# Kernel tuning notes

Hardware: AMD Instinct MI355X
Metric: run time of the kernel (lower is better)

## Reference

```python
import jax, jax.numpy as jnp
import numpy as np

B, N, F_IN, F_OUT = 16, 1024, 256, 256
ALPHA = 0.2  # leakyrelu negative slope
NEG_BIG = -9e15


def setup_inputs() -> dict:
    key = jax.random.key(0)
    k1, k2, k3, k4 = jax.random.split(key, 4)
    h = jax.random.normal(k1, (B, N, F_IN), dtype=jnp.float32)
    adj = jax.random.randint(k2, (B, N, N), 0, 2, dtype=jnp.int32)
    # xavier_uniform with gain=1.414
    def xavier(k, shape, gain=1.414):
        fan_in, fan_out = shape[0], shape[1]
        bound = gain * np.sqrt(6.0 / (fan_in + fan_out))
        return jax.random.uniform(k, shape, dtype=jnp.float32, minval=-bound, maxval=bound)
    W = xavier(k3, (F_IN, F_OUT))
    a = xavier(k4, (2 * F_OUT, 1))
    return {"h": h, "adj": adj, "W": W, "a": a}


def reference(h, adj, W, a):
    Wh = jnp.matmul(h, W)  # [B, N, F_OUT]
    # a^T [Wh_i ; Wh_j] = a1^T Wh_i + a2^T Wh_j -- avoids O(N^2 * 2F) concat tensor
    a1 = a[:F_OUT, 0]  # [F_OUT]
    a2 = a[F_OUT:, 0]  # [F_OUT]
    e_i = jnp.einsum('bnf,f->bn', Wh, a1)  # score contribution of source node i
    e_j = jnp.einsum('bnf,f->bn', Wh, a2)  # score contribution of target node j
    e = e_i[:, :, None] + e_j[:, None, :]  # [B, N, N]
    e = jnp.where(e > 0, e, ALPHA * e)  # leaky relu
    e = jnp.where(adj > 0, e, NEG_BIG)
    attention = jax.nn.softmax(e, axis=2)
    h_prime = jnp.matmul(attention, Wh)  # [B, N, F_OUT]
    return jax.nn.elu(h_prime)  # concat=True
```

## Files before the change

### kernel.cpp

```cpp
#include <hip/hip_runtime.h>
#include <hip/hip_bf16.h>

#define B_ 16
#define N_ 1024
#define F_ 256
#define ALPHA 0.2f
#define NEG_BIG -9.0e15f
#define LOG2E 1.4426950408889634f

typedef float f4 __attribute__((ext_vector_type(4)));
typedef float f32x4 __attribute__((ext_vector_type(4)));
typedef short s16x8 __attribute__((ext_vector_type(8)));
typedef short s16x4 __attribute__((ext_vector_type(4)));

__device__ inline short f2bs(float x) {
    __hip_bfloat16 h = __float2bfloat16(x);
    return __builtin_bit_cast(short, h);
}

__global__ __launch_bounds__(256) void k_pre(const float* __restrict__ W,
                                             const float* __restrict__ a,
                                             float* __restrict__ wa,
                                             unsigned short* __restrict__ WTb) {
    const int t = threadIdx.x, lane = t & 63, w = t >> 6;
    if (blockIdx.x < 64) {
        const int row = blockIdx.x * 4 + w;
        const f4 wv = *(const f4*)(W + (size_t)row * F_ + lane * 4);
        const f4 a1 = *(const f4*)(a + lane * 4);
        const f4 a2 = *(const f4*)(a + F_ + lane * 4);
        float s1 = wv[0]*a1[0] + wv[1]*a1[1] + wv[2]*a1[2] + wv[3]*a1[3];
        float s2 = wv[0]*a2[0] + wv[1]*a2[1] + wv[2]*a2[2] + wv[3]*a2[3];
#pragma unroll
        for (int off = 32; off > 0; off >>= 1) {
            s1 += __shfl_xor(s1, off);
            s2 += __shfl_xor(s2, off);
        }
        if (lane == 0) { wa[row] = s1; wa[256 + row] = s2; }
    } else {
        __shared__ float tile[64][65];
        const int wb = blockIdx.x - 64;
        const int k0 = (wb >> 2) * 64, f0 = (wb & 3) * 64;
#pragma unroll
        for (int rep = 0; rep < 4; ++rep) {
            const int idx = rep * 256 + t;
            const int kr = idx >> 4, fc = (idx & 15) * 4;
            const f4 v = *(const f4*)(W + (size_t)(k0 + kr) * F_ + f0 + fc);
            tile[kr][fc] = v[0]; tile[kr][fc + 1] = v[1];
            tile[kr][fc + 2] = v[2]; tile[kr][fc + 3] = v[3];
        }
        __syncthreads();
#pragma unroll
        for (int rep = 0; rep < 4; ++rep) {
            const int idx = rep * 256 + t;
            const int fr = idx >> 4, kc = (idx & 15) * 4;
            s16x4 v;
            v[0] = f2bs(tile[kc][fr]);     v[1] = f2bs(tile[kc + 1][fr]);
            v[2] = f2bs(tile[kc + 2][fr]); v[3] = f2bs(tile[kc + 3][fr]);
            *(s16x4*)(WTb + (size_t)(f0 + fr) * F_ + k0 + kc) = v;
        }
    }
}

__global__ __launch_bounds__(256, 4) void k_big(const float* __restrict__ h,
                                                const unsigned short* __restrict__ WTb,
                                                const float* __restrict__ wa,
                                                const int* __restrict__ adj,
                                                unsigned short* __restrict__ WhT,
                                                float* __restrict__ ei,
                                                float* __restrict__ ej,
                                                unsigned long long* __restrict__ mask) {
    const int bid = blockIdx.x;
    const int t = threadIdx.x, l = t & 63, w = t >> 6;
    if (bid < 2048) {
        const int gw = bid * 4 + w;
#pragma unroll
        for (int rr = 0; rr < 2; ++rr) {
            const int row = gw + rr * 8192;
            const int* ar = adj + (size_t)row * 1024;
            int v[16];
#pragma unroll
            for (int g = 0; g < 16; ++g) v[g] = ar[g * 64 + l];
            unsigned long long myw = 0;
#pragma unroll
            for (int g = 0; g < 16; ++g) {
                const unsigned long long bal = __ballot(v[g] > 0);
                if (l == g) myw = bal;
            }
            if (l < 16) mask[(size_t)row * 16 + l] = myw;
        }
    } else if (bid < 2560) {
        const int m0 = (bid - 2048) * 32;
        const int ih = w >> 1, fh = w & 1;
        const int li = l & 15, jg = l >> 4;
        const int mrow = m0 + ih * 16 + li;
        const float* hrow = h + (size_t)mrow * F_ + jg * 8;
        const unsigned short* bbase = WTb + (size_t)(fh * 128 + li) * F_ + jg * 8;
        f32x4 acc[8] = {};
#pragma unroll
        for (int kk = 0; kk < 8; ++kk) {
            const f4 lo = *(const f4*)(hrow + kk * 32);
            const f4 hi = *(const f4*)(hrow + kk * 32 + 4);
            s16x8 av;
            av[0]=f2bs(lo[0]); av[1]=f2bs(lo[1]); av[2]=f2bs(lo[2]); av[3]=f2bs(lo[3]);
            av[4]=f2bs(hi[0]); av[5]=f2bs(hi[1]); av[6]=f2bs(hi[2]); av[7]=f2bs(hi[3]);
#pragma unroll
            for (int ft = 0; ft < 8; ++ft) {
                const s16x8 bv = *(const s16x8*)(bbase + (size_t)ft * 16 * F_ + kk * 32);
                acc[ft] = __builtin_amdgcn_mfma_f32_16x16x32_bf16(av, bv, acc[ft], 0, 0, 0);
            }
        }
        const int bb = m0 >> 10;
        const int mb = (m0 & 1023) + ih * 16 + jg * 4;
#pragma unroll
        for (int ft = 0; ft < 8; ++ft) {
            const int fg = fh * 128 + ft * 16 + li;
            s16x4 v;
            v[0]=f2bs(acc[ft][0]); v[1]=f2bs(acc[ft][1]);
            v[2]=f2bs(acc[ft][2]); v[3]=f2bs(acc[ft][3]);
            *(s16x4*)(WhT + ((size_t)(bb * 256 + fg)) * 1024 + mb) = v;
        }
    } else {
        const int row = (bid - 2560) * 4 + w;
        const f4 hv = *(const f4*)(h + (size_t)row * F_ + l * 4);
        const f4 w1 = *(const f4*)(wa + l * 4);
        const f4 w2 = *(const f4*)(wa + 256 + l * 4);
        float s1 = hv[0]*w1[0] + hv[1]*w1[1] + hv[2]*w1[2] + hv[3]*w1[3];
        float s2 = hv[0]*w2[0] + hv[1]*w2[1] + hv[2]*w2[2] + hv[3]*w2[3];
#pragma unroll
        for (int off = 32; off > 0; off >>= 1) {
            s1 += __shfl_xor(s1, off);
            s2 += __shfl_xor(s2, off);
        }
        if (l == 0) { ei[row] = s1 * LOG2E; ej[row] = s2 * LOG2E; }
    }
}

__global__ __launch_bounds__(256, 2) void k_attn(const unsigned short* __restrict__ WhT,
                                                 const float* __restrict__ ei_g,
                                                 const float* __restrict__ ej_g,
                                                 const unsigned long long* __restrict__ mask,
                                                 float* __restrict__ out) {
    const int id = blockIdx.x;
    const int xcd = id & 7, slot = id >> 3;
    const int b = xcd * 2 + (slot >> 5);
    const int i0 = (slot & 31) * 32;

    const int t = threadIdx.x, l = t & 63, w = t >> 6;
    const int fbase = w * 64;
    const int li = l & 15, jg = l >> 4;

    const unsigned short* whb = WhT + (size_t)b * F_ * N_;
    const float* ejb = ej_g + b * N_;
    const float ei0 = ei_g[b * N_ + i0 + li];
    const float ei1 = ei_g[b * N_ + i0 + 16 + li];
    const unsigned long long* mrow0 = mask + (size_t)(b * N_ + i0 + li) * 16;
    const unsigned long long* mrow1 = mrow0 + 256;

    const unsigned short* bptr[4];
#pragma unroll
    for (int ft = 0; ft < 4; ++ft)
        bptr[ft] = whb + (size_t)(fbase + ft * 16 + li) * N_ + jg * 8;

    float m0 = NEG_BIG, m1 = NEG_BIG, ll0 = 0.f, ll1 = 0.f;
    f32x4 acc0[4] = {}, acc1[4] = {};

    for (int s = 0; s < 16; ++s) {
        const unsigned long long w0 = mrow0[s], w1 = mrow1[s];
        const int jb = s * 64 + jg * 8;
        const f4 ejA = *(const f4*)(ejb + jb);
        const f4 ejB = *(const f4*)(ejb + jb + 4);
        const f4 ejC = *(const f4*)(ejb + jb + 32);
        const f4 ejD = *(const f4*)(ejb + jb + 36);
        s16x8 bv0[4], bv1[4];
#pragma unroll
        for (int ft = 0; ft < 4; ++ft) {
            bv0[ft] = *(const s16x8*)(bptr[ft] + s * 64);
            bv1[ft] = *(const s16x8*)(bptr[ft] + s * 64 + 32);
        }
#pragma unroll
        for (int sub = 0; sub < 2; ++sub) {
            const f4 eja = sub ? ejC : ejA;
            const f4 ejbv = sub ? ejD : ejB;
            const unsigned int ms0 = (unsigned int)(w0 >> (sub * 32 + jg * 8));
            const unsigned int ms1 = (unsigned int)(w1 >> (sub * 32 + jg * 8));
            float p0[8], p1[8];
            float tm0 = NEG_BIG, tm1 = NEG_BIG;
#pragma unroll
            for (int e = 0; e < 8; ++e) {
                const float ejv = (e < 4) ? eja[e] : ejbv[e - 4];
                float s0 = ei0 + ejv;
                s0 = fmaxf(s0, ALPHA * s0);
                p0[e] = s0; tm0 = fmaxf(tm0, s0);
                float s1 = ei1 + ejv;
                s1 = fmaxf(s1, ALPHA * s1);
                p1[e] = s1; tm1 = fmaxf(tm1, s1);
            }
            tm0 = fmaxf(tm0, __shfl_xor(tm0, 16));
            tm0 = fmaxf(tm0, __shfl_xor(tm0, 32));
            tm1 = fmaxf(tm1, __shfl_xor(tm1, 16));
            tm1 = fmaxf(tm1, __shfl_xor(tm1, 32));
            if (__any(tm0 > m0 + 11.5f)) {
                const float mn = fmaxf(m0, tm0);
                const float fac = __builtin_amdgcn_exp2f(m0 - mn);
                m0 = mn; ll0 *= fac;
                float fr[4];
#pragma unroll
                for (int q = 0; q < 4; ++q) fr[q] = __shfl(fac, jg * 4 + q);
#pragma unroll
                for (int ft = 0; ft < 4; ++ft)
#pragma unroll
                    for (int q = 0; q < 4; ++q) acc0[ft][q] *= fr[q];
            }
            if (__any(tm1 > m1 + 11.5f)) {
                const float mn = fmaxf(m1, tm1);
                const float fac = __builtin_amdgcn_exp2f(m1 - mn);
                m1 = mn; ll1 *= fac;
                float fr[4];
#pragma unroll
                for (int q = 0; q < 4; ++q) fr[q] = __shfl(fac, jg * 4 + q);
#pragma unroll
                for (int ft = 0; ft < 4; ++ft)
#pragma unroll
                    for (int q = 0; q < 4; ++q) acc1[ft][q] *= fr[q];
            }
            float sum0 = 0.f, sum1 = 0.f;
            s16x8 af0, af1;
#pragma unroll
            for (int e = 0; e < 8; ++e) {
                const float b0 = (float)((ms0 >> e) & 1u);
                const float b1 = (float)((ms1 >> e) & 1u);
                const float pe0 = __builtin_amdgcn_exp2f(p0[e] - m0) * b0;
                const float pe1 = __builtin_amdgcn_exp2f(p1[e] - m1) * b1;
                af0[e] = f2bs(pe0); sum0 += pe0;
                af1[e] = f2bs(pe1); sum1 += pe1;
            }
            sum0 += __shfl_xor(sum0, 16); sum0 += __shfl_xor(sum0, 32);
            sum1 += __shfl_xor(sum1, 16); sum1 += __shfl_xor(sum1, 32);
            ll0 += sum0; ll1 += sum1;
            const s16x8* bv = sub ? bv1 : bv0;
#pragma unroll
            for (int ft = 0; ft < 4; ++ft) {
                acc0[ft] = __builtin_amdgcn_mfma_f32_16x16x32_bf16(af0, bv[ft], acc0[ft], 0, 0, 0);
                acc1[ft] = __builtin_amdgcn_mfma_f32_16x16x32_bf16(af1, bv[ft], acc1[ft], 0, 0, 0);
            }
        }
    }

    const float il0 = 1.f / ll0, il1 = 1.f / ll1;
    float inv0[4], inv1[4];
#pragma unroll
    for (int q = 0; q < 4; ++q) {
        inv0[q] = __shfl(il0, jg * 4 + q);
        inv1[q] = __shfl(il1, jg * 4 + q);
    }
#pragma unroll
    for (int ft = 0; ft < 4; ++ft) {
#pragma unroll
        for (int q = 0; q < 4; ++q) {
            float v0 = acc0[ft][q] * inv0[q];
            v0 = v0 > 0.f ? v0 : __builtin_amdgcn_exp2f(v0 * LOG2E) - 1.f;
            out[((size_t)b * N_ + i0 + jg * 4 + q) * F_ + fbase + ft * 16 + li] = v0;
            float v1 = acc1[ft][q] * inv1[q];
            v1 = v1 > 0.f ? v1 : __builtin_amdgcn_exp2f(v1 * LOG2E) - 1.f;
            out[((size_t)b * N_ + i0 + 16 + jg * 4 + q) * F_ + fbase + ft * 16 + li] = v1;
        }
    }
}

extern "C" void kernel_launch(void* const* d_in, const int* in_sizes, int n_in,
                              void* d_out, int out_size, void* d_ws, size_t ws_size,
                              hipStream_t stream) {
    const float* h = (const float*)d_in[0];
    const int* adj = (const int*)d_in[1];
    const float* W = (const float*)d_in[2];
    const float* a = (const float*)d_in[3];
    float* out = (float*)d_out;

    unsigned short* WhT = (unsigned short*)d_ws;
    float* wa = (float*)(WhT + (size_t)B_ * N_ * F_);
    float* ei = wa + 512;
    float* ej = ei + (size_t)B_ * N_;
    unsigned short* WTb = (unsigned short*)(ej + (size_t)B_ * N_);
    unsigned long long* mask = (unsigned long long*)(WTb + 65536);

    k_pre<<<80, 256, 0, stream>>>(W, a, wa, WTb);
    k_big<<<6656, 256, 0, stream>>>(h, WTb, wa, adj, WhT, ei, ej, mask);
    k_attn<<<512, 256, 0, stream>>>(WhT, ei, ej, mask, out);
}
```

Measured before the change: 188.2 us.

## Split softmax scoring across waves and share probabilities through LDS

The attention kernel now handles 16 query rows per block instead of 32, with twice as many blocks and a higher occupancy target. Each wave now computes scores, masked exponentials and row sums for 4 of the 16 rows rather than every wave redundantly computing all rows. The bf16 probability tile and the rescale factors are exchanged through shared memory before the MFMA accumulation. In exchange it adds two block barriers per 64-column step, rescales the accumulator unconditionally, and reloads WhT from global memory twice as often, since each block now covers fewer rows.

After: 202.6 us. 7.7% more time.

```diff
diff --git a/kernel.cpp b/kernel.cpp
--- a/kernel.cpp
+++ b/kernel.cpp
@@ -135,134 +135,105 @@
     }
 }
 
-__global__ __launch_bounds__(256, 2) void k_attn(const unsigned short* __restrict__ WhT,
+__global__ __launch_bounds__(256, 4) void k_attn(const unsigned short* __restrict__ WhT,
                                                  const float* __restrict__ ei_g,
                                                  const float* __restrict__ ej_g,
                                                  const unsigned long long* __restrict__ mask,
                                                  float* __restrict__ out) {
     const int id = blockIdx.x;
     const int xcd = id & 7, slot = id >> 3;
-    const int b = xcd * 2 + (slot >> 5);
-    const int i0 = (slot & 31) * 32;
+    const int b = xcd * 2 + (slot >> 6);
+    const int i0 = (slot & 63) * 16;
+
+    __shared__ unsigned short P_lds[16][72];
+    __shared__ __align__(16) float sF[16];
 
     const int t = threadIdx.x, l = t & 63, w = t >> 6;
+    const int li = l & 15, jg = l >> 4;
     const int fbase = w * 64;
-    const int li = l & 15, jg = l >> 4;
+
+    const int orow = w * 4 + jg;
+    const float eival = ei_g[b * N_ + i0 + orow];
+    const unsigned long long* mrow = mask + (size_t)(b * N_ + i0 + orow) * 16;
+    const float* ejb = ej_g + b * N_;
 
     const unsigned short* whb = WhT + (size_t)b * F_ * N_;
-    const float* ejb = ej_g + b * N_;
-    const float ei0 = ei_g[b * N_ + i0 + li];
-    const float ei1 = ei_g[b * N_ + i0 + 16 + li];
-    const unsigned long long* mrow0 = mask + (size_t)(b * N_ + i0 + li) * 16;
-    const unsigned long long* mrow1 = mrow0 + 256;
-
     const unsigned short* bptr[4];
 #pragma unroll
     for (int ft = 0; ft < 4; ++ft)
         bptr[ft] = whb + (size_t)(fbase + ft * 16 + li) * N_ + jg * 8;
 
-    float m0 = NEG_BIG, m1 = NEG_BIG, ll0 = 0.f, ll1 = 0.f;
-    f32x4 acc0[4] = {}, acc1[4] = {};
+    float m = NEG_BIG, ll = 0.f;
+    f32x4 acc[4] = {};
 
     for (int s = 0; s < 16; ++s) {
-        const unsigned long long w0 = mrow0[s], w1 = mrow1[s];
-        const int jb = s * 64 + jg * 8;
-        const f4 ejA = *(const f4*)(ejb + jb);
-        const f4 ejB = *(const f4*)(ejb + jb + 4);
-        const f4 ejC = *(const f4*)(ejb + jb + 32);
-        const f4 ejD = *(const f4*)(ejb + jb + 36);
         s16x8 bv0[4], bv1[4];
 #pragma unroll
         for (int ft = 0; ft < 4; ++ft) {
             bv0[ft] = *(const s16x8*)(bptr[ft] + s * 64);
             bv1[ft] = *(const s16x8*)(bptr[ft] + s * 64 + 32);
         }
-#pragma unroll
-        for (int sub = 0; sub < 2; ++sub) {
-            const f4 eja = sub ? ejC : ejA;
-            const f4 ejbv = sub ? ejD : ejB;
-            const unsigned int ms0 = (unsigned int)(w0 >> (sub * 32 + jg * 8));
-            const unsigned int ms1 = (unsigned int)(w1 >> (sub * 32 + jg * 8));
-            float p0[8], p1[8];
-            float tm0 = NEG_BIG, tm1 = NEG_BIG;
-#pragma unroll
-            for (int e = 0; e < 8; ++e) {
-                const float ejv = (e < 4) ? eja[e] : ejbv[e - 4];
-                float s0 = ei0 + ejv;
-                s0 = fmaxf(s0, ALPHA * s0);
-                p0[e] = s0; tm0 = fmaxf(tm0, s0);
-                float s1 = ei1 + ejv;
-                s1 = fmaxf(s1, ALPHA * s1);
-                p1[e] = s1; tm1 = fmaxf(tm1, s1);
-            }
-            tm0 = fmaxf(tm0, __shfl_xor(tm0, 16));
-            tm0 = fmaxf(tm0, __shfl_xor(tm0, 32));
-            tm1 = fmaxf(tm1, __shfl_xor(tm1, 16));
-            tm1 = fmaxf(tm1, __shfl_xor(tm1, 32));
-            if (__any(tm0 > m0 + 11.5f)) {
-                const float mn = fmaxf(m0, tm0);
-                const float fac = __builtin_amdgcn_exp2f(m0 - mn);
-                m0 = mn; ll0 *= fac;
-                float fr[4];
-#pragma unroll
-                for (int q = 0; q < 4; ++q) fr[q] = __shfl(fac, jg * 4 + q);
-#pragma unroll
-                for (int ft = 0; ft < 4; ++ft)
-#pragma unroll
-                    for (int q = 0; q < 4; ++q) acc0[ft][q] *= fr[q];
-            }
-            if (__any(tm1 > m1 + 11.5f)) {
-                const float mn = fmaxf(m1, tm1);
-                const float fac = __builtin_amdgcn_exp2f(m1 - mn);
-                m1 = mn; ll1 *= fac;
-                float fr[4];
-#pragma unroll
-                for (int q = 0; q < 4; ++q) fr[q] = __shfl(fac, jg * 4 + q);
-#pragma unroll
-                for (int ft = 0; ft < 4; ++ft)
-#pragma unroll
-                    for (int q = 0; q < 4; ++q) acc1[ft][q] *= fr[q];
-            }
-            float sum0 = 0.f, sum1 = 0.f;
-            s16x8 af0, af1;
-#pragma unroll
-            for (int e = 0; e < 8; ++e) {
-                const float b0 = (float)((ms0 >> e) & 1u);
-                const float b1 = (float)((ms1 >> e) & 1u);
-                const float pe0 = __builtin_amdgcn_exp2f(p0[e] - m0) * b0;
-                const float pe1 = __builtin_amdgcn_exp2f(p1[e] - m1) * b1;
-                af0[e] = f2bs(pe0); sum0 += pe0;
-                af1[e] = f2bs(pe1); sum1 += pe1;
-            }
-            sum0 += __shfl_xor(sum0, 16); sum0 += __shfl_xor(sum0, 32);
-            sum1 += __shfl_xor(sum1, 16); sum1 += __shfl_xor(sum1, 32);
-            ll0 += sum0; ll1 += sum1;
-            const s16x8* bv = sub ? bv1 : bv0;
-#pragma unroll
-            for (int ft = 0; ft < 4; ++ft) {
-                acc0[ft] = __builtin_amdgcn_mfma_f32_16x16x32_bf16(af0, bv[ft], acc0[ft], 0, 0, 0);
-                acc1[ft] = __builtin_amdgcn_mfma_f32_16x16x32_bf16(af1, bv[ft], acc1[ft], 0, 0, 0);
-            }
-        }
-    }
-
-    const float il0 = 1.f / ll0, il1 = 1.f / ll1;
-    float inv0[4], inv1[4];
-#pragma unroll
-    for (int q = 0; q < 4; ++q) {
-        inv0[q] = __shfl(il0, jg * 4 + q);
-        inv1[q] = __shfl(il1, jg * 4 + q);
-    }
+        const unsigned long long w0 = mrow[s];
+        const f4 ejv = *(const f4*)(ejb + s * 64 + li * 4);
+
+        float p[4];
+        float tm = NEG_BIG;
+#pragma unroll
+        for (int e = 0; e < 4; ++e) {
+            float sc = eival + ejv[e];
+            sc = fmaxf(sc, ALPHA * sc);
+            p[e] = sc;
+            tm = fmaxf(tm, sc);
+        }
+        tm = fmaxf(tm, __shfl_xor(tm, 1));
+        tm = fmaxf(tm, __shfl_xor(tm, 2));
+        tm = fmaxf(tm, __shfl_xor(tm, 4));
+        tm = fmaxf(tm, __shfl_xor(tm, 8));
+        const float mn = fmaxf(m, tm);
+        const float fac = __builtin_amdgcn_exp2f(m - mn);
+        m = mn;
+        const unsigned int bits = (unsigned int)(w0 >> (li * 4)) & 0xFu;
+        float sum = 0.f;
+        s16x4 pw;
+#pragma unroll
+        for (int e = 0; e < 4; ++e) {
+            const float pe = __builtin_amdgcn_exp2f(p[e] - m) *
+                             (float)((bits >> e) & 1u);
+            pw[e] = f2bs(pe);
+            sum += pe;
+        }
+        sum += __shfl_xor(sum, 1);
+        sum += __shfl_xor(sum, 2);
+        sum += __shfl_xor(sum, 4);
+        sum += __shfl_xor(sum, 8);
+        ll = ll * fac + sum;
+        if (li == 0) sF[orow] = fac;
+        *(s16x4*)&P_lds[orow][li * 4] = pw;
+        __syncthreads();
+
+        const f4 frv = *(const f4*)&sF[jg * 4];
+        const s16x8 pa0 = *(const s16x8*)&P_lds[li][jg * 8];
+        const s16x8 pa1 = *(const s16x8*)&P_lds[li][32 + jg * 8];
+#pragma unroll
+        for (int ft = 0; ft < 4; ++ft) {
+#pragma unroll
+            for (int q = 0; q < 4; ++q) acc[ft][q] *= frv[q];
+            acc[ft] = __builtin_amdgcn_mfma_f32_16x16x32_bf16(pa0, bv0[ft], acc[ft], 0, 0, 0);
+            acc[ft] = __builtin_amdgcn_mfma_f32_16x16x32_bf16(pa1, bv1[ft], acc[ft], 0, 0, 0);
+        }
+        __syncthreads();
+    }
+
+    if (li == 0) sF[orow] = 1.f / ll;
+    __syncthreads();
+    const f4 invv = *(const f4*)&sF[jg * 4];
 #pragma unroll
     for (int ft = 0; ft < 4; ++ft) {
 #pragma unroll
         for (int q = 0; q < 4; ++q) {
-            float v0 = acc0[ft][q] * inv0[q];
-            v0 = v0 > 0.f ? v0 : __builtin_amdgcn_exp2f(v0 * LOG2E) - 1.f;
-            out[((size_t)b * N_ + i0 + jg * 4 + q) * F_ + fbase + ft * 16 + li] = v0;
-            float v1 = acc1[ft][q] * inv1[q];
-            v1 = v1 > 0.f ? v1 : __builtin_amdgcn_exp2f(v1 * LOG2E) - 1.f;
-            out[((size_t)b * N_ + i0 + 16 + jg * 4 + q) * F_ + fbase + ft * 16 + li] = v1;
+            float v = acc[ft][q] * invv[q];
+            v = v > 0.f ? v : __builtin_amdgcn_exp2f(v * LOG2E) - 1.f;
+            out[((size_t)b * N_ + i0 + jg * 4 + q) * F_ + fbase + ft * 16 + li] = v;
         }
     }
 }
@@ -285,5 +256,5 @@
 
     k_pre<<<80, 256, 0, stream>>>(W, a, wa, WTb);
     k_big<<<6656, 256, 0, stream>>>(h, WTb, wa, adj, WhT, ei, ej, mask);
-    k_attn<<<512, 256, 0, stream>>>(WhT, ei, ej, mask, out);
-}
+    k_attn<<<1024, 256, 0, stream>>>(WhT, ei, ej, mask, out);
+}
```
